# Performance work log

Hardware: AMD Instinct MI355X
Metric: run time of the kernel (lower is better)

## Reference

```python
import jax, jax.numpy as jnp
import numpy as np

B, S, H, NH = 2, 2048, 1024, 16
D = H // NH
EPS = 1.1920929e-07  # torch fp32 finfo eps used by F.rms_norm default
ROPE_BASE = 10000.0


def setup_inputs() -> dict:
    key = jax.random.key(0)
    k0, k1, k2, k3 = jax.random.split(key, 4)
    return {
        "x": jax.random.normal(k0, (B, S, H), jnp.float32),
        "ve": jax.random.normal(k1, (B, S, H), jnp.float32),
        "W_qkv": jax.random.normal(k2, (3 * H, H), jnp.float32) * 0.02,
        "W_o": jax.random.normal(k3, (H, H), jnp.float32) * 0.02,
        "lambdas": jnp.array([0.5, 0.5], jnp.float32),
    }


def _rms_norm(x):
    # F.rms_norm without learnable weight, over last dim
    return x * jax.lax.rsqrt(jnp.mean(x * x, axis=-1, keepdims=True) + EPS)


def _rope(x):
    # x: [b, s, h, d]; rotate-half style RoPE matching the Rotary module
    d = x.shape[-1]
    inv_freq = (1.0 / ROPE_BASE) ** (jnp.arange(0, d, 2, dtype=jnp.float32) / d)
    t = jnp.arange(x.shape[1], dtype=jnp.float32)
    freqs = t[:, None] * inv_freq[None, :]          # [s, d/2]
    cos = jnp.cos(freqs)[None, :, None, :]
    sin = jnp.sin(freqs)[None, :, None, :]
    x1, x2 = jnp.split(x, 2, axis=-1)
    return jnp.concatenate([x1 * cos + x2 * sin, -x1 * sin + x2 * cos], axis=-1)


def reference(x, ve, W_qkv, W_o, lambdas):
    qkv = x @ W_qkv.T                                # [b, s, 3H]
    q, k, v = jnp.split(qkv, 3, axis=-1)
    rs = lambda a: a.reshape(B, S, NH, D)            # b s (h d) -> b s h d
    q, k, v = rs(q), rs(k), rs(v)
    q = _rope(_rms_norm(q))
    k = _rope(_rms_norm(k))
    v = lambdas[0] * v + lambdas[1] * rs(ve)         # value-lambda mix
    scale = 1.0 / jnp.sqrt(jnp.asarray(D, jnp.float32))  # flex_attention default
    scores = jnp.einsum('bqhd,bkhd->bhqk', q, k) * scale
    causal = jnp.tril(jnp.ones((S, S), bool))
    scores = jnp.where(causal[None, None], scores, jnp.asarray(-jnp.inf, scores.dtype))
    p = jax.nn.softmax(scores, axis=-1)
    a = jnp.einsum('bhqk,bkhd->bqhd', p, v).reshape(B, S, H)
    return a @ W_o.T
```

## Files before the change

kernel.cpp:

```cpp
#include <hip/hip_runtime.h>
#include <math.h>

typedef __bf16 bf16;
typedef __attribute__((ext_vector_type(8))) __bf16 bf16x8;
typedef __attribute__((ext_vector_type(4))) __bf16 bf16x4;
typedef __attribute__((ext_vector_type(4))) float f32x4;

#define B_  2
#define S_  2048
#define H_  1024
#define NH_ 16
#define D_  64

__device__ __forceinline__ f32x4 mfma16(bf16x8 a, bf16x8 b, f32x4 c) {
    return __builtin_amdgcn_mfma_f32_16x16x32_bf16(a, b, c, 0, 0, 0);
}

__device__ __forceinline__ void async16(void* lds, const void* g) {
    __builtin_amdgcn_global_load_lds(
        (const __attribute__((address_space(1))) unsigned int*)g,
        (__attribute__((address_space(3))) unsigned int*)lds, 16, 0, 0);
}

__global__ __launch_bounds__(256) void cvt_main(
    const float* __restrict__ x, const float* __restrict__ wqkv,
    bf16* __restrict__ xb, bf16* __restrict__ wqb, float2* __restrict__ tab)
{
    const int bid = blockIdx.x, tid = threadIdx.x;
    if (bid < 4096) {
        int i = bid * 256 + tid;
        f32x4 v = *(const f32x4*)(x + (size_t)i * 4);
        bf16x4 o; o[0]=(bf16)v[0]; o[1]=(bf16)v[1]; o[2]=(bf16)v[2]; o[3]=(bf16)v[3];
        *(bf16x4*)(xb + (size_t)i * 4) = o;
    } else if (bid < 7168) {
        int i = (bid - 4096) * 256 + tid;
        f32x4 v = *(const f32x4*)(wqkv + (size_t)i * 4);
        bf16x4 o; o[0]=(bf16)v[0]; o[1]=(bf16)v[1]; o[2]=(bf16)v[2]; o[3]=(bf16)v[3];
        *(bf16x4*)(wqb + (size_t)i * 4) = o;
    } else {
        int idx = (bid - 7168) * 256 + tid;
        int s = idx >> 5, i = idx & 31;
        float f = exp2f((float)i * (-13.287712379549449f / 32.0f));
        float sn, cs;
        sincosf((float)s * f, &sn, &cs);
        tab[idx] = make_float2(cs, sn);
    }
}

__global__ __launch_bounds__(256) void cvt_bf16(const float* __restrict__ src,
                                                bf16* __restrict__ dst, int n4) {
    int i = blockIdx.x * 256 + threadIdx.x;
    if (i >= n4) return;
    f32x4 v = *(const f32x4*)(src + (size_t)i * 4);
    bf16x4 o; o[0]=(bf16)v[0]; o[1]=(bf16)v[1]; o[2]=(bf16)v[2]; o[3]=(bf16)v[3];
    *(bf16x4*)(dst + (size_t)i * 4) = o;
}

template <int EPI, int NT>
__global__ __launch_bounds__(256) void gemm_bt(
    const bf16* __restrict__ A, const bf16* __restrict__ W,
    int M, int N, int K,
    float* __restrict__ outF,
    bf16* __restrict__ qb, bf16* __restrict__ kb, bf16* __restrict__ vtb,
    const float* __restrict__ ve, const float* __restrict__ lambdas,
    const float2* __restrict__ tab)
{
    constexpr int JN = NT / 32;
    __shared__ bf16 Al[128][64];
    __shared__ bf16 Bl[NT][64];
    const int m0   = blockIdx.y * 128;
    const int n0   = blockIdx.x * NT;
    const int tid  = threadIdx.x;
    const int lane = tid & 63;
    const int w    = tid >> 6;
    const int quad = lane >> 4;
    const int l16  = lane & 15;
    const int wm   = (w >> 1) * 64;
    const int wn   = (w & 1) * (NT / 2);
    const int r8   = lane >> 3;
    const int cs   = ((lane & 7) ^ r8) * 8;

    const f32x4 Z4 = {0.f, 0.f, 0.f, 0.f};
    f32x4 acc[4][JN];
#pragma unroll
    for (int i = 0; i < 4; ++i)
#pragma unroll
        for (int j = 0; j < JN; ++j) acc[i][j] = Z4;

    for (int k0 = 0; k0 < K; k0 += 64) {
        {
            const bf16* gA = A + (size_t)(m0 + w * 32 + r8) * K + k0 + cs;
            async16(&Al[w * 32][0],      gA);
            async16(&Al[w * 32 + 8][0],  gA + (size_t)8  * K);
            async16(&Al[w * 32 + 16][0], gA + (size_t)16 * K);
            async16(&Al[w * 32 + 24][0], gA + (size_t)24 * K);
        }
        if constexpr (NT == 128) {
            const bf16* gB = W + (size_t)(n0 + w * 32 + r8) * K + k0 + cs;
            async16(&Bl[w * 32][0],      gB);
            async16(&Bl[w * 32 + 8][0],  gB + (size_t)8  * K);
            async16(&Bl[w * 32 + 16][0], gB + (size_t)16 * K);
            async16(&Bl[w * 32 + 24][0], gB + (size_t)24 * K);
        } else {
            const bf16* gB = W + (size_t)(n0 + w * 16 + r8) * K + k0 + cs;
            async16(&Bl[w * 16][0],     gB);
            async16(&Bl[w * 16 + 8][0], gB + (size_t)8 * K);
        }
        __syncthreads();
#pragma unroll
        for (int ks = 0; ks < 2; ++ks) {
            bf16x8 af[4], bfg[JN];
#pragma unroll
            for (int i = 0; i < 4; ++i)
                af[i] = *(const bf16x8*)
                    &Al[wm + i * 16 + l16][(((ks << 2) + quad) ^ (l16 & 7)) * 8];
#pragma unroll
            for (int j = 0; j < JN; ++j)
                bfg[j] = *(const bf16x8*)
                    &Bl[wn + j * 16 + l16][(((ks << 2) + quad) ^ (l16 & 7)) * 8];
#pragma unroll
            for (int i = 0; i < 4; ++i)
#pragma unroll
                for (int j = 0; j < JN; ++j)
                    acc[i][j] = mfma16(af[i], bfg[j], acc[i][j]);
        }
        __syncthreads();
    }

    if constexpr (EPI == 1) {
#pragma unroll
        for (int i = 0; i < 4; ++i)
#pragma unroll
            for (int j = 0; j < JN; ++j)
#pragma unroll
                for (int r = 0; r < 4; ++r) {
                    int m = m0 + wm + i * 16 + quad * 4 + r;
                    int n = n0 + wn + j * 16 + l16;
                    outF[(size_t)m * N + n] = acc[i][j][r];
                }
    } else {
        const int nbase = n0 + wn;
        const int which = nbase >> 10;
        const int h     = (nbase & (H_ - 1)) >> 6;
        if (which < 2) {
            bf16* dst = which ? kb : qb;
#pragma unroll
            for (int i = 0; i < 4; ++i) {
                float ss[4];
#pragma unroll
                for (int r = 0; r < 4; ++r)
                    ss[r] = acc[i][0][r] * acc[i][0][r] + acc[i][1][r] * acc[i][1][r]
                          + acc[i][2][r] * acc[i][2][r] + acc[i][3][r] * acc[i][3][r];
#pragma unroll
                for (int r = 0; r < 4; ++r) {
                    ss[r] += __shfl_xor(ss[r], 1);
                    ss[r] += __shfl_xor(ss[r], 2);
                    ss[r] += __shfl_xor(ss[r], 4);
                    ss[r] += __shfl_xor(ss[r], 8);
                }
#pragma unroll
                for (int r = 0; r < 4; ++r) {
                    int    m   = m0 + wm + i * 16 + quad * 4 + r;
                    int    bb  = m >> 11, s = m & (S_ - 1);
                    float  rms = rsqrtf(ss[r] * (1.0f / 64.0f) + 1.1920929e-07f);
                    float  x0 = acc[i][0][r] * rms, x1 = acc[i][1][r] * rms;
                    float  x2 = acc[i][2][r] * rms, x3 = acc[i][3][r] * rms;
                    float2 t0 = tab[(size_t)s * 32 + l16];
                    float2 t1 = tab[(size_t)s * 32 + 16 + l16];
                    bf16*  bp = dst + ((size_t)(bb * NH_ + h) * S_ + s) * D_;
                    bp[l16]      = (bf16)(x0 * t0.x + x2 * t0.y);
                    bp[16 + l16] = (bf16)(x1 * t1.x + x3 * t1.y);
                    bp[32 + l16] = (bf16)(x2 * t0.x - x0 * t0.y);
                    bp[48 + l16] = (bf16)(x3 * t1.x - x1 * t1.y);
                }
            }
        } else {
            const float l0 = lambdas[0], l1 = lambdas[1];
#pragma unroll
            for (int i = 0; i < 4; ++i) {
                const int m00 = m0 + wm + i * 16 + quad * 4;
                const int bb  = m00 >> 11, s = m00 & (S_ - 1);
#pragma unroll
                for (int j = 0; j < 4; ++j) {
                    const int d = j * 16 + l16;
                    bf16x4 pk;
#pragma unroll
                    for (int r = 0; r < 4; ++r) {
                        float vm = l0 * acc[i][j][r]
                                 + l1 * ve[(size_t)(m00 + r) * H_ + h * 64 + d];
                        pk[r] = (bf16)vm;
                    }
                    *(bf16x4*)&vtb[((size_t)(bb * NH_ + h) * D_ + d) * S_ + s] = pk;
                }
            }
        }
    }
}

__global__ __launch_bounds__(256) void attn(
    const bf16* __restrict__ Q, const bf16* __restrict__ Kg,
    const bf16* __restrict__ Vt, bf16* __restrict__ Og)
{
    __shared__ bf16 Kl[2][64][64];
    __shared__ bf16 Vl[2][64][64];
    __shared__ bf16 Pl[4][16][64];

    const int bh   = blockIdx.y;
    const int b    = bh >> 4;
    const int h    = bh & 15;
    const int tid  = threadIdx.x;
    const int lane = tid & 63;
    const int w    = tid >> 6;
    const int quad = lane >> 4;
    const int l16  = lane & 15;
    const int l7   = l16 & 7;

    const bf16* Qp = Q  + (size_t)bh * S_ * D_;
    const bf16* Kp = Kg + (size_t)bh * S_ * D_;
    const bf16* Vp = Vt + (size_t)bh * D_ * S_;

    const int srow = lane >> 3;
    const int schk = (lane & 7) ^ (lane >> 3);
    const f32x4 Z4 = {0.f, 0.f, 0.f, 0.f};
    const float C1 = 0.18033688011112042f;
    const float C2 = -11.541560327111707f;

    auto stage = [&](int p, int kb0) {
        const bf16* gK = Kp + (size_t)(kb0 + w * 16 + srow) * D_ + schk * 8;
        async16(&Kl[p][w * 16][0], gK);
        async16(&Kl[p][w * 16 + 8][0], gK + (size_t)8 * D_);
        const bf16* gV = Vp + (size_t)(w * 16 + srow) * S_ + kb0 + schk * 8;
        async16(&Vl[p][w * 16][0], gV);
        async16(&Vl[p][w * 16 + 8][0], gV + (size_t)8 * S_);
    };

    for (int half = 0; half < 2; ++half) {
        const int qt    = half ? (31 - blockIdx.x) : blockIdx.x;
        const int qbase = qt * 64 + w * 16;
        const int qi    = qbase + l16;

        bf16x8 qf0 = *(const bf16x8*)(Qp + (size_t)(qbase + l16) * D_ + quad * 8);
        bf16x8 qf1 = *(const bf16x8*)(Qp + (size_t)(qbase + l16) * D_ + 32 + quad * 8);

        f32x4 of[4];
#pragma unroll
        for (int dt = 0; dt < 4; ++dt) of[dt] = Z4;
        float lsum = 0.f;

        const int nch = qt + 1;
        __syncthreads();
        stage(0, 0);
        for (int c = 0; c < nch; ++c) {
            const int p   = c & 1;
            const int kb0 = c * 64;
            __syncthreads();
            if (c + 1 < nch) stage(p ^ 1, kb0 + 64);

            float ps = 0.f;
            if (c < qt) {
#pragma unroll
                for (int nt = 0; nt < 4; ++nt) {
                    bf16x8 kf0 = *(const bf16x8*)&Kl[p][nt * 16 + l16][(quad ^ l7) * 8];
                    bf16x8 kf1 = *(const bf16x8*)&Kl[p][nt * 16 + l16][((quad + 4) ^ l7) * 8];
                    f32x4 sacc = Z4;
                    sacc = mfma16(kf0, qf0, sacc);
                    sacc = mfma16(kf1, qf1, sacc);
                    bf16x4 pk;
#pragma unroll
                    for (int r = 0; r < 4; ++r) {
                        float pv = exp2f(fmaf(sacc[r], C1, C2));
                        ps += pv;
                        pk[r] = (bf16)pv;
                    }
                    *(bf16x4*)&Pl[w][l16][((nt * 2 + (quad >> 1)) ^ l7) * 8 + (quad & 1) * 4] = pk;
                }
            } else {
#pragma unroll
                for (int nt = 0; nt < 4; ++nt) {
                    bf16x8 kf0 = *(const bf16x8*)&Kl[p][nt * 16 + l16][(quad ^ l7) * 8];
                    bf16x8 kf1 = *(const bf16x8*)&Kl[p][nt * 16 + l16][((quad + 4) ^ l7) * 8];
                    f32x4 sacc = Z4;
                    sacc = mfma16(kf0, qf0, sacc);
                    sacc = mfma16(kf1, qf1, sacc);
                    bf16x4 pk;
#pragma unroll
                    for (int r = 0; r < 4; ++r) {
                        int   key = kb0 + nt * 16 + quad * 4 + r;
                        float pv  = (key <= qi) ? exp2f(fmaf(sacc[r], C1, C2)) : 0.f;
                        ps += pv;
                        pk[r] = (bf16)pv;
                    }
                    *(bf16x4*)&Pl[w][l16][((nt * 2 + (quad >> 1)) ^ l7) * 8 + (quad & 1) * 4] = pk;
                }
            }
            ps += __shfl_xor(ps, 16);
            ps += __shfl_xor(ps, 32);
            lsum += ps;

            bf16x8 pf0 = *(const bf16x8*)&Pl[w][l16][(quad ^ l7) * 8];
            bf16x8 pf1 = *(const bf16x8*)&Pl[w][l16][((quad + 4) ^ l7) * 8];
#pragma unroll
            for (int dt = 0; dt < 4; ++dt) {
                bf16x8 vf0 = *(const bf16x8*)&Vl[p][dt * 16 + l16][(quad ^ l7) * 8];
                bf16x8 vf1 = *(const bf16x8*)&Vl[p][dt * 16 + l16][((quad + 4) ^ l7) * 8];
                of[dt] = mfma16(pf0, vf0, of[dt]);
                of[dt] = mfma16(pf1, vf1, of[dt]);
            }
        }

#pragma unroll
        for (int r = 0; r < 4; ++r) {
            float ld = __shfl(lsum, quad * 4 + r);
            float rl = 1.0f / ld;
            int   qq = qbase + quad * 4 + r;
#pragma unroll
            for (int dt = 0; dt < 4; ++dt)
                Og[((size_t)(b * S_ + qq)) * H_ + h * D_ + dt * 16 + l16] =
                    (bf16)(of[dt][r] * rl);
        }
    }
}

extern "C" void kernel_launch(void* const* d_in, const int* in_sizes, int n_in,
                              void* d_out, int out_size, void* d_ws, size_t ws_size,
                              hipStream_t stream)
{
    const float* x       = (const float*)d_in[0];
    const float* ve      = (const float*)d_in[1];
    const float* Wqkv    = (const float*)d_in[2];
    const float* Wo      = (const float*)d_in[3];
    const float* lambdas = (const float*)d_in[4];
    float* out = (float*)d_out;

    char* od = (char*)d_out;
    char* ws = (char*)d_ws;
    const size_t MB = 1024 * 1024;
    bf16*   xb  = (bf16*)(od);
    bf16*   wqb = (bf16*)(od + 8 * MB);
    float2* tab = (float2*)(od + 14 * MB);
    bf16*   qb  = (bf16*)(ws);
    bf16*   kb  = (bf16*)(ws + 8 * MB);
    bf16*   vtb = (bf16*)(ws + 16 * MB);
    bf16*   ao  = (bf16*)(ws + 24 * MB);
    bf16*   wob = (bf16*)(ws);

    cvt_main<<<7424, 256, 0, stream>>>(x, Wqkv, xb, wqb, tab);
    gemm_bt<0, 128><<<dim3(24, 32), 256, 0, stream>>>(
        xb, wqb, B_ * S_, 3 * H_, H_, nullptr, qb, kb, vtb, ve, lambdas, (const float2*)tab);
    attn<<<dim3(16, B_ * NH_), 256, 0, stream>>>(qb, kb, vtb, ao);
    cvt_bf16<<<1024, 256, 0, stream>>>(Wo, wob, (H_ * H_) / 4);
    gemm_bt<1, 64><<<dim3(16, 32), 256, 0, stream>>>(
        ao, wob, B_ * S_, H_, H_, out, nullptr, nullptr, nullptr, nullptr, nullptr, nullptr);
}
```

Before: 208.1 us.

## Double-buffer GEMM K loop and fuse W_o fp32-to-bf16 conversion into output GEMM

Restructures the GEMM main loop to use two 32-wide K stages in LDS, prefetching the next tile while MFMAs run on the current one, with one barrier per iteration instead of two. The output projection GEMM now reads W_o in fp32 directly, converts it to bf16 in registers and stores it to LDS, which removes the separate conversion kernel launch. This trades a smaller K-step per iteration and redundant per-block W_o conversion for fewer barriers, load/compute overlap and one fewer launch.

```diff
diff --git a/kernel.cpp b/kernel.cpp
--- a/kernel.cpp
+++ b/kernel.cpp
@@ -47,18 +47,10 @@
     }
 }
 
-__global__ __launch_bounds__(256) void cvt_bf16(const float* __restrict__ src,
-                                                bf16* __restrict__ dst, int n4) {
-    int i = blockIdx.x * 256 + threadIdx.x;
-    if (i >= n4) return;
-    f32x4 v = *(const f32x4*)(src + (size_t)i * 4);
-    bf16x4 o; o[0]=(bf16)v[0]; o[1]=(bf16)v[1]; o[2]=(bf16)v[2]; o[3]=(bf16)v[3];
-    *(bf16x4*)(dst + (size_t)i * 4) = o;
-}
-
 template <int EPI, int NT>
 __global__ __launch_bounds__(256) void gemm_bt(
     const bf16* __restrict__ A, const bf16* __restrict__ W,
+    const float* __restrict__ Wf,
     int M, int N, int K,
     float* __restrict__ outF,
     bf16* __restrict__ qb, bf16* __restrict__ kb, bf16* __restrict__ vtb,
@@ -66,8 +58,8 @@
     const float2* __restrict__ tab)
 {
     constexpr int JN = NT / 32;
-    __shared__ bf16 Al[128][64];
-    __shared__ bf16 Bl[NT][64];
+    __shared__ bf16 Al[2][128][32];
+    __shared__ bf16 Bl[2][NT][32];
     const int m0   = blockIdx.y * 128;
     const int n0   = blockIdx.x * NT;
     const int tid  = threadIdx.x;
@@ -77,8 +69,10 @@
     const int l16  = lane & 15;
     const int wm   = (w >> 1) * 64;
     const int wn   = (w & 1) * (NT / 2);
-    const int r8   = lane >> 3;
-    const int cs   = ((lane & 7) ^ r8) * 8;
+    const int g    = lane >> 2;
+    const int achk = (lane & 3) ^ (g & 3) ^ (g >> 2);
+    const int br   = tid >> 2;
+    const int bphy = (tid & 3) ^ (br & 3) ^ ((br >> 2) & 3);
 
     const f32x4 Z4 = {0.f, 0.f, 0.f, 0.f};
     f32x4 acc[4][JN];
@@ -87,44 +81,65 @@
 #pragma unroll
         for (int j = 0; j < JN; ++j) acc[i][j] = Z4;
 
-    for (int k0 = 0; k0 < K; k0 += 64) {
-        {
-            const bf16* gA = A + (size_t)(m0 + w * 32 + r8) * K + k0 + cs;
-            async16(&Al[w * 32][0],      gA);
-            async16(&Al[w * 32 + 8][0],  gA + (size_t)8  * K);
-            async16(&Al[w * 32 + 16][0], gA + (size_t)16 * K);
-            async16(&Al[w * 32 + 24][0], gA + (size_t)24 * K);
-        }
-        if constexpr (NT == 128) {
-            const bf16* gB = W + (size_t)(n0 + w * 32 + r8) * K + k0 + cs;
-            async16(&Bl[w * 32][0],      gB);
-            async16(&Bl[w * 32 + 8][0],  gB + (size_t)8  * K);
-            async16(&Bl[w * 32 + 16][0], gB + (size_t)16 * K);
-            async16(&Bl[w * 32 + 24][0], gB + (size_t)24 * K);
-        } else {
-            const bf16* gB = W + (size_t)(n0 + w * 16 + r8) * K + k0 + cs;
-            async16(&Bl[w * 16][0],     gB);
-            async16(&Bl[w * 16 + 8][0], gB + (size_t)8 * K);
-        }
+    auto stageA = [&](int p, int k0) {
+        const bf16* gA = A + (size_t)(m0 + w * 32 + g) * K + k0 + achk * 8;
+        async16(&Al[p][w * 32][0],      gA);
+        async16(&Al[p][w * 32 + 16][0], gA + (size_t)16 * K);
+    };
+    auto stageB = [&](int p, int k0) {
+        const bf16* gB = W + (size_t)(n0 + w * 32 + g) * K + k0 + achk * 8;
+        async16(&Bl[p][w * 32][0],      gB);
+        async16(&Bl[p][w * 32 + 16][0], gB + (size_t)16 * K);
+    };
+
+    const int niter = K >> 5;
+    stageA(0, 0);
+    if constexpr (EPI == 0) stageB(0, 0);
+    else {
+        const float* src = Wf + (size_t)(n0 + br) * K + (tid & 3) * 8;
+        f32x4 f0 = *(const f32x4*)(src);
+        f32x4 f1 = *(const f32x4*)(src + 4);
+        bf16x8 v;
+#pragma unroll
+        for (int q = 0; q < 4; ++q) { v[q] = (bf16)f0[q]; v[4 + q] = (bf16)f1[q]; }
+        *(bf16x8*)&Bl[0][br][bphy * 8] = v;
+    }
+
+    const int fsw = (l16 & 3) ^ (l16 >> 2);
+    for (int c = 0; c < niter; ++c) {
+        const int p = c & 1;
         __syncthreads();
-#pragma unroll
-        for (int ks = 0; ks < 2; ++ks) {
-            bf16x8 af[4], bfg[JN];
-#pragma unroll
-            for (int i = 0; i < 4; ++i)
-                af[i] = *(const bf16x8*)
-                    &Al[wm + i * 16 + l16][(((ks << 2) + quad) ^ (l16 & 7)) * 8];
+        const int k1 = (c + 1) << 5;
+        f32x4 f0, f1;
+        if (c + 1 < niter) {
+            stageA(p ^ 1, k1);
+            if constexpr (EPI == 0) stageB(p ^ 1, k1);
+            else {
+                const float* src = Wf + (size_t)(n0 + br) * K + k1 + (tid & 3) * 8;
+                f0 = *(const f32x4*)(src);
+                f1 = *(const f32x4*)(src + 4);
+            }
+        }
+        bf16x8 af[4], bfg[JN];
+#pragma unroll
+        for (int i = 0; i < 4; ++i)
+            af[i] = *(const bf16x8*)&Al[p][wm + i * 16 + l16][(quad ^ fsw) * 8];
+#pragma unroll
+        for (int j = 0; j < JN; ++j)
+            bfg[j] = *(const bf16x8*)&Bl[p][wn + j * 16 + l16][(quad ^ fsw) * 8];
+#pragma unroll
+        for (int i = 0; i < 4; ++i)
 #pragma unroll
             for (int j = 0; j < JN; ++j)
-                bfg[j] = *(const bf16x8*)
-                    &Bl[wn + j * 16 + l16][(((ks << 2) + quad) ^ (l16 & 7)) * 8];
-#pragma unroll
-            for (int i = 0; i < 4; ++i)
-#pragma unroll
-                for (int j = 0; j < JN; ++j)
-                    acc[i][j] = mfma16(af[i], bfg[j], acc[i][j]);
-        }
-        __syncthreads();
+                acc[i][j] = mfma16(af[i], bfg[j], acc[i][j]);
+        if constexpr (EPI == 1) {
+            if (c + 1 < niter) {
+                bf16x8 v;
+#pragma unroll
+                for (int q = 0; q < 4; ++q) { v[q] = (bf16)f0[q]; v[4 + q] = (bf16)f1[q]; }
+                *(bf16x8*)&Bl[p ^ 1][br][bphy * 8] = v;
+            }
+        }
     }
 
     if constexpr (EPI == 1) {
@@ -342,13 +357,13 @@
     bf16*   kb  = (bf16*)(ws + 8 * MB);
     bf16*   vtb = (bf16*)(ws + 16 * MB);
     bf16*   ao  = (bf16*)(ws + 24 * MB);
-    bf16*   wob = (bf16*)(ws);
 
     cvt_main<<<7424, 256, 0, stream>>>(x, Wqkv, xb, wqb, tab);
     gemm_bt<0, 128><<<dim3(24, 32), 256, 0, stream>>>(
-        xb, wqb, B_ * S_, 3 * H_, H_, nullptr, qb, kb, vtb, ve, lambdas, (const float2*)tab);
+        xb, wqb, nullptr, B_ * S_, 3 * H_, H_, nullptr, qb, kb, vtb, ve, lambdas,
+        (const float2*)tab);
     attn<<<dim3(16, B_ * NH_), 256, 0, stream>>>(qb, kb, vtb, ao);
-    cvt_bf16<<<1024, 256, 0, stream>>>(Wo, wob, (H_ * H_) / 4);
     gemm_bt<1, 64><<<dim3(16, 32), 256, 0, stream>>>(
-        ao, wob, B_ * S_, H_, H_, out, nullptr, nullptr, nullptr, nullptr, nullptr, nullptr);
-}
+        ao, nullptr, Wo, B_ * S_, H_, H_, out, nullptr, nullptr, nullptr,
+        nullptr, nullptr, nullptr);
+}
```

Result: slower. 222.1 us (+6.7%).

## Fuse W_o bf16 conversion into output GEMM and double query tile per attention block

Applied to the files above, without the earlier changes.

Removes the standalone W_o conversion kernel by loading fp32 W_o tiles into registers inside the output-projection GEMM, converting them to bf16 and storing them into swizzled LDS, with the next tile prefetched after the barrier. The attention kernel now processes 128 query rows per block as two 64-row sub-tiles sharing each staged K/V chunk, halving K/V LDS staging per query. This halves the attention grid, reducing parallelism to one block per CU, and adds per-element mask checks on all chunks.

```diff
diff --git a/kernel.cpp b/kernel.cpp
--- a/kernel.cpp
+++ b/kernel.cpp
@@ -47,18 +47,10 @@
     }
 }
 
-__global__ __launch_bounds__(256) void cvt_bf16(const float* __restrict__ src,
-                                                bf16* __restrict__ dst, int n4) {
-    int i = blockIdx.x * 256 + threadIdx.x;
-    if (i >= n4) return;
-    f32x4 v = *(const f32x4*)(src + (size_t)i * 4);
-    bf16x4 o; o[0]=(bf16)v[0]; o[1]=(bf16)v[1]; o[2]=(bf16)v[2]; o[3]=(bf16)v[3];
-    *(bf16x4*)(dst + (size_t)i * 4) = o;
-}
-
 template <int EPI, int NT>
 __global__ __launch_bounds__(256) void gemm_bt(
     const bf16* __restrict__ A, const bf16* __restrict__ W,
+    const float* __restrict__ Wf,
     int M, int N, int K,
     float* __restrict__ outF,
     bf16* __restrict__ qb, bf16* __restrict__ kb, bf16* __restrict__ vtb,
@@ -79,6 +71,8 @@
     const int wn   = (w & 1) * (NT / 2);
     const int r8   = lane >> 3;
     const int cs   = ((lane & 7) ^ r8) * 8;
+    const int tr   = tid >> 2;
+    const int c2   = (tid & 3) * 2;
 
     const f32x4 Z4 = {0.f, 0.f, 0.f, 0.f};
     f32x4 acc[4][JN];
@@ -87,7 +81,18 @@
 #pragma unroll
         for (int j = 0; j < JN; ++j) acc[i][j] = Z4;
 
-    for (int k0 = 0; k0 < K; k0 += 64) {
+    f32x4 wreg[4];
+    if constexpr (EPI == 1) {
+        const float* src = Wf + (size_t)(n0 + tr) * K + c2 * 8;
+        wreg[0] = *(const f32x4*)(src);
+        wreg[1] = *(const f32x4*)(src + 4);
+        wreg[2] = *(const f32x4*)(src + 8);
+        wreg[3] = *(const f32x4*)(src + 12);
+    }
+
+    const int niter = K >> 6;
+    for (int it = 0; it < niter; ++it) {
+        const int k0 = it << 6;
         {
             const bf16* gA = A + (size_t)(m0 + w * 32 + r8) * K + k0 + cs;
             async16(&Al[w * 32][0],      gA);
@@ -95,18 +100,32 @@
             async16(&Al[w * 32 + 16][0], gA + (size_t)16 * K);
             async16(&Al[w * 32 + 24][0], gA + (size_t)24 * K);
         }
-        if constexpr (NT == 128) {
+        if constexpr (EPI == 0) {
             const bf16* gB = W + (size_t)(n0 + w * 32 + r8) * K + k0 + cs;
             async16(&Bl[w * 32][0],      gB);
             async16(&Bl[w * 32 + 8][0],  gB + (size_t)8  * K);
             async16(&Bl[w * 32 + 16][0], gB + (size_t)16 * K);
             async16(&Bl[w * 32 + 24][0], gB + (size_t)24 * K);
         } else {
-            const bf16* gB = W + (size_t)(n0 + w * 16 + r8) * K + k0 + cs;
-            async16(&Bl[w * 16][0],     gB);
-            async16(&Bl[w * 16 + 8][0], gB + (size_t)8 * K);
+            bf16x8 v0, v1;
+#pragma unroll
+            for (int q = 0; q < 4; ++q) {
+                v0[q] = (bf16)wreg[0][q]; v0[4 + q] = (bf16)wreg[1][q];
+                v1[q] = (bf16)wreg[2][q]; v1[4 + q] = (bf16)wreg[3][q];
+            }
+            *(bf16x8*)&Bl[tr][(c2 ^ (tr & 7)) * 8]       = v0;
+            *(bf16x8*)&Bl[tr][((c2 + 1) ^ (tr & 7)) * 8] = v1;
         }
         __syncthreads();
+        if constexpr (EPI == 1) {
+            if (it + 1 < niter) {
+                const float* src = Wf + (size_t)(n0 + tr) * K + k0 + 64 + c2 * 8;
+                wreg[0] = *(const f32x4*)(src);
+                wreg[1] = *(const f32x4*)(src + 4);
+                wreg[2] = *(const f32x4*)(src + 8);
+                wreg[3] = *(const f32x4*)(src + 12);
+            }
+        }
 #pragma unroll
         for (int ks = 0; ks < 2; ++ks) {
             bf16x8 af[4], bfg[JN];
@@ -235,19 +254,27 @@
     };
 
     for (int half = 0; half < 2; ++half) {
-        const int qt    = half ? (31 - blockIdx.x) : blockIdx.x;
-        const int qbase = qt * 64 + w * 16;
-        const int qi    = qbase + l16;
-
-        bf16x8 qf0 = *(const bf16x8*)(Qp + (size_t)(qbase + l16) * D_ + quad * 8);
-        bf16x8 qf1 = *(const bf16x8*)(Qp + (size_t)(qbase + l16) * D_ + 32 + quad * 8);
-
-        f32x4 of[4];
-#pragma unroll
-        for (int dt = 0; dt < 4; ++dt) of[dt] = Z4;
-        float lsum = 0.f;
-
-        const int nch = qt + 1;
+        const int qt    = half ? (15 - blockIdx.x) : blockIdx.x;
+        const int qbase = qt * 128;
+
+        bf16x8 qf[2][2];
+        int    qi[2];
+#pragma unroll
+        for (int qs = 0; qs < 2; ++qs) {
+            int qr = qbase + qs * 64 + w * 16 + l16;
+            qi[qs] = qr;
+            qf[qs][0] = *(const bf16x8*)(Qp + (size_t)qr * D_ + quad * 8);
+            qf[qs][1] = *(const bf16x8*)(Qp + (size_t)qr * D_ + 32 + quad * 8);
+        }
+
+        f32x4 of[2][4];
+#pragma unroll
+        for (int qs = 0; qs < 2; ++qs)
+#pragma unroll
+            for (int dt = 0; dt < 4; ++dt) of[qs][dt] = Z4;
+        float lsum[2] = {0.f, 0.f};
+
+        const int nch = 2 * qt + 2;
         __syncthreads();
         stage(0, 0);
         for (int c = 0; c < nch; ++c) {
@@ -256,68 +283,56 @@
             __syncthreads();
             if (c + 1 < nch) stage(p ^ 1, kb0 + 64);
 
-            float ps = 0.f;
-            if (c < qt) {
+#pragma unroll
+            for (int qs = 0; qs < 2; ++qs) {
+                if (qs == 0 && c == 2 * qt + 1) continue;
+                const int klim = (c == 2 * qt + qs) ? qi[qs] : 0x7fffffff;
+                float ps = 0.f;
 #pragma unroll
                 for (int nt = 0; nt < 4; ++nt) {
                     bf16x8 kf0 = *(const bf16x8*)&Kl[p][nt * 16 + l16][(quad ^ l7) * 8];
                     bf16x8 kf1 = *(const bf16x8*)&Kl[p][nt * 16 + l16][((quad + 4) ^ l7) * 8];
                     f32x4 sacc = Z4;
-                    sacc = mfma16(kf0, qf0, sacc);
-                    sacc = mfma16(kf1, qf1, sacc);
+                    sacc = mfma16(kf0, qf[qs][0], sacc);
+                    sacc = mfma16(kf1, qf[qs][1], sacc);
                     bf16x4 pk;
 #pragma unroll
                     for (int r = 0; r < 4; ++r) {
-                        float pv = exp2f(fmaf(sacc[r], C1, C2));
+                        int   key = kb0 + nt * 16 + quad * 4 + r;
+                        float pv  = (key <= klim) ? exp2f(fmaf(sacc[r], C1, C2)) : 0.f;
                         ps += pv;
                         pk[r] = (bf16)pv;
                     }
                     *(bf16x4*)&Pl[w][l16][((nt * 2 + (quad >> 1)) ^ l7) * 8 + (quad & 1) * 4] = pk;
                 }
-            } else {
-#pragma unroll
-                for (int nt = 0; nt < 4; ++nt) {
-                    bf16x8 kf0 = *(const bf16x8*)&Kl[p][nt * 16 + l16][(quad ^ l7) * 8];
-                    bf16x8 kf1 = *(const bf16x8*)&Kl[p][nt * 16 + l16][((quad + 4) ^ l7) * 8];
-                    f32x4 sacc = Z4;
-                    sacc = mfma16(kf0, qf0, sacc);
-                    sacc = mfma16(kf1, qf1, sacc);
-                    bf16x4 pk;
-#pragma unroll
-                    for (int r = 0; r < 4; ++r) {
-                        int   key = kb0 + nt * 16 + quad * 4 + r;
-                        float pv  = (key <= qi) ? exp2f(fmaf(sacc[r], C1, C2)) : 0.f;
-                        ps += pv;
-                        pk[r] = (bf16)pv;
-                    }
-                    *(bf16x4*)&Pl[w][l16][((nt * 2 + (quad >> 1)) ^ l7) * 8 + (quad & 1) * 4] = pk;
-                }
-            }
-            ps += __shfl_xor(ps, 16);
-            ps += __shfl_xor(ps, 32);
-            lsum += ps;
-
-            bf16x8 pf0 = *(const bf16x8*)&Pl[w][l16][(quad ^ l7) * 8];
-            bf16x8 pf1 = *(const bf16x8*)&Pl[w][l16][((quad + 4) ^ l7) * 8];
-#pragma unroll
-            for (int dt = 0; dt < 4; ++dt) {
-                bf16x8 vf0 = *(const bf16x8*)&Vl[p][dt * 16 + l16][(quad ^ l7) * 8];
-                bf16x8 vf1 = *(const bf16x8*)&Vl[p][dt * 16 + l16][((quad + 4) ^ l7) * 8];
-                of[dt] = mfma16(pf0, vf0, of[dt]);
-                of[dt] = mfma16(pf1, vf1, of[dt]);
-            }
-        }
-
-#pragma unroll
-        for (int r = 0; r < 4; ++r) {
-            float ld = __shfl(lsum, quad * 4 + r);
-            float rl = 1.0f / ld;
-            int   qq = qbase + quad * 4 + r;
-#pragma unroll
-            for (int dt = 0; dt < 4; ++dt)
-                Og[((size_t)(b * S_ + qq)) * H_ + h * D_ + dt * 16 + l16] =
-                    (bf16)(of[dt][r] * rl);
-        }
+                ps += __shfl_xor(ps, 16);
+                ps += __shfl_xor(ps, 32);
+                lsum[qs] += ps;
+
+                bf16x8 pf0 = *(const bf16x8*)&Pl[w][l16][(quad ^ l7) * 8];
+                bf16x8 pf1 = *(const bf16x8*)&Pl[w][l16][((quad + 4) ^ l7) * 8];
+#pragma unroll
+                for (int dt = 0; dt < 4; ++dt) {
+                    bf16x8 vf0 = *(const bf16x8*)&Vl[p][dt * 16 + l16][(quad ^ l7) * 8];
+                    bf16x8 vf1 = *(const bf16x8*)&Vl[p][dt * 16 + l16][((quad + 4) ^ l7) * 8];
+                    of[qs][dt] = mfma16(pf0, vf0, of[qs][dt]);
+                    of[qs][dt] = mfma16(pf1, vf1, of[qs][dt]);
+                }
+            }
+        }
+
+#pragma unroll
+        for (int qs = 0; qs < 2; ++qs)
+#pragma unroll
+            for (int r = 0; r < 4; ++r) {
+                float ld = __shfl(lsum[qs], quad * 4 + r);
+                float rl = 1.0f / ld;
+                int   qq = qbase + qs * 64 + w * 16 + quad * 4 + r;
+#pragma unroll
+                for (int dt = 0; dt < 4; ++dt)
+                    Og[((size_t)(b * S_ + qq)) * H_ + h * D_ + dt * 16 + l16] =
+                        (bf16)(of[qs][dt][r] * rl);
+            }
     }
 }
 
@@ -342,13 +357,13 @@
     bf16*   kb  = (bf16*)(ws + 8 * MB);
     bf16*   vtb = (bf16*)(ws + 16 * MB);
     bf16*   ao  = (bf16*)(ws + 24 * MB);
-    bf16*   wob = (bf16*)(ws);
 
     cvt_main<<<7424, 256, 0, stream>>>(x, Wqkv, xb, wqb, tab);
     gemm_bt<0, 128><<<dim3(24, 32), 256, 0, stream>>>(
-        xb, wqb, B_ * S_, 3 * H_, H_, nullptr, qb, kb, vtb, ve, lambdas, (const float2*)tab);
-    attn<<<dim3(16, B_ * NH_), 256, 0, stream>>>(qb, kb, vtb, ao);
-    cvt_bf16<<<1024, 256, 0, stream>>>(Wo, wob, (H_ * H_) / 4);
+        xb, wqb, nullptr, B_ * S_, 3 * H_, H_, nullptr, qb, kb, vtb, ve, lambdas,
+        (const float2*)tab);
+    attn<<<dim3(8, B_ * NH_), 256, 0, stream>>>(qb, kb, vtb, ao);
     gemm_bt<1, 64><<<dim3(16, 32), 256, 0, stream>>>(
-        ao, wob, B_ * S_, H_, H_, out, nullptr, nullptr, nullptr, nullptr, nullptr, nullptr);
-}
+        ao, nullptr, Wo, B_ * S_, H_, H_, out, nullptr, nullptr, nullptr,
+        nullptr, nullptr, nullptr);
+}
```

Result: slower. 232.9 us (+11.9%).

## Split attention key range across two blocks and add a combine kernel

Applied to the files above, without the earlier changes.

Splits each query tile's causal key range into two halves handled by separate blocks (split-K attention). This doubles the attention grid from 512 to 1024 blocks to improve occupancy across the CUs. The unnormalized partial outputs and row sums are written to scratch buffers, then summed and normalized by a new combine kernel. Because the softmax uses a fixed offset rather than a running max, the partials add directly. The cost is an extra launch and extra global traffic for the partial outputs, and the partials are rounded to bf16 before being combined.

```diff
diff --git a/kernel.cpp b/kernel.cpp
--- a/kernel.cpp
+++ b/kernel.cpp
@@ -199,13 +199,15 @@
 
 __global__ __launch_bounds__(256) void attn(
     const bf16* __restrict__ Q, const bf16* __restrict__ Kg,
-    const bf16* __restrict__ Vt, bf16* __restrict__ Og)
+    const bf16* __restrict__ Vt, bf16* __restrict__ opart,
+    float* __restrict__ lsumg)
 {
     __shared__ bf16 Kl[2][64][64];
     __shared__ bf16 Vl[2][64][64];
     __shared__ bf16 Pl[4][16][64];
 
-    const int bh   = blockIdx.y;
+    const int sz   = blockIdx.y;
+    const int bh   = blockIdx.z;
     const int b    = bh >> 4;
     const int h    = bh & 15;
     const int tid  = threadIdx.x;
@@ -218,6 +220,8 @@
     const bf16* Qp = Q  + (size_t)bh * S_ * D_;
     const bf16* Kp = Kg + (size_t)bh * S_ * D_;
     const bf16* Vp = Vt + (size_t)bh * D_ * S_;
+    bf16*  op = opart + (size_t)sz * (B_ * S_ * H_);
+    float* lp = lsumg + sz * (B_ * NH_ * S_);
 
     const int srow = lane >> 3;
     const int schk = (lane & 7) ^ (lane >> 3);
@@ -238,6 +242,10 @@
         const int qt    = half ? (31 - blockIdx.x) : blockIdx.x;
         const int qbase = qt * 64 + w * 16;
         const int qi    = qbase + l16;
+        const int nt    = qt + 1;
+        const int h0    = (nt + 1) >> 1;
+        const int c0    = sz ? h0 : 0;
+        const int c1    = sz ? nt : h0;
 
         bf16x8 qf0 = *(const bf16x8*)(Qp + (size_t)(qbase + l16) * D_ + quad * 8);
         bf16x8 qf1 = *(const bf16x8*)(Qp + (size_t)(qbase + l16) * D_ + 32 + quad * 8);
@@ -247,78 +255,82 @@
         for (int dt = 0; dt < 4; ++dt) of[dt] = Z4;
         float lsum = 0.f;
 
-        const int nch = qt + 1;
-        __syncthreads();
-        stage(0, 0);
-        for (int c = 0; c < nch; ++c) {
-            const int p   = c & 1;
-            const int kb0 = c * 64;
+        if (c0 < c1) {
             __syncthreads();
-            if (c + 1 < nch) stage(p ^ 1, kb0 + 64);
-
-            float ps = 0.f;
-            if (c < qt) {
-#pragma unroll
-                for (int nt = 0; nt < 4; ++nt) {
-                    bf16x8 kf0 = *(const bf16x8*)&Kl[p][nt * 16 + l16][(quad ^ l7) * 8];
-                    bf16x8 kf1 = *(const bf16x8*)&Kl[p][nt * 16 + l16][((quad + 4) ^ l7) * 8];
+            stage(0, c0 * 64);
+            for (int c = c0; c < c1; ++c) {
+                const int p   = (c - c0) & 1;
+                const int kb0 = c * 64;
+                __syncthreads();
+                if (c + 1 < c1) stage(p ^ 1, kb0 + 64);
+
+                const int klim = (c == nt - 1) ? qi : 0x7fffffff;
+                float ps = 0.f;
+#pragma unroll
+                for (int ntl = 0; ntl < 4; ++ntl) {
+                    bf16x8 kf0 = *(const bf16x8*)&Kl[p][ntl * 16 + l16][(quad ^ l7) * 8];
+                    bf16x8 kf1 = *(const bf16x8*)&Kl[p][ntl * 16 + l16][((quad + 4) ^ l7) * 8];
                     f32x4 sacc = Z4;
                     sacc = mfma16(kf0, qf0, sacc);
                     sacc = mfma16(kf1, qf1, sacc);
                     bf16x4 pk;
 #pragma unroll
                     for (int r = 0; r < 4; ++r) {
-                        float pv = exp2f(fmaf(sacc[r], C1, C2));
+                        int   key = kb0 + ntl * 16 + quad * 4 + r;
+                        float pv  = (key <= klim) ? exp2f(fmaf(sacc[r], C1, C2)) : 0.f;
                         ps += pv;
                         pk[r] = (bf16)pv;
                     }
-                    *(bf16x4*)&Pl[w][l16][((nt * 2 + (quad >> 1)) ^ l7) * 8 + (quad & 1) * 4] = pk;
-                }
-            } else {
-#pragma unroll
-                for (int nt = 0; nt < 4; ++nt) {
-                    bf16x8 kf0 = *(const bf16x8*)&Kl[p][nt * 16 + l16][(quad ^ l7) * 8];
-                    bf16x8 kf1 = *(const bf16x8*)&Kl[p][nt * 16 + l16][((quad + 4) ^ l7) * 8];
-                    f32x4 sacc = Z4;
-                    sacc = mfma16(kf0, qf0, sacc);
-                    sacc = mfma16(kf1, qf1, sacc);
-                    bf16x4 pk;
-#pragma unroll
-                    for (int r = 0; r < 4; ++r) {
-                        int   key = kb0 + nt * 16 + quad * 4 + r;
-                        float pv  = (key <= qi) ? exp2f(fmaf(sacc[r], C1, C2)) : 0.f;
-                        ps += pv;
-                        pk[r] = (bf16)pv;
-                    }
-                    *(bf16x4*)&Pl[w][l16][((nt * 2 + (quad >> 1)) ^ l7) * 8 + (quad & 1) * 4] = pk;
+                    *(bf16x4*)&Pl[w][l16][((ntl * 2 + (quad >> 1)) ^ l7) * 8 + (quad & 1) * 4] = pk;
+                }
+                ps += __shfl_xor(ps, 16);
+                ps += __shfl_xor(ps, 32);
+                lsum += ps;
+
+                bf16x8 pf0 = *(const bf16x8*)&Pl[w][l16][(quad ^ l7) * 8];
+                bf16x8 pf1 = *(const bf16x8*)&Pl[w][l16][((quad + 4) ^ l7) * 8];
+#pragma unroll
+                for (int dt = 0; dt < 4; ++dt) {
+                    bf16x8 vf0 = *(const bf16x8*)&Vl[p][dt * 16 + l16][(quad ^ l7) * 8];
+                    bf16x8 vf1 = *(const bf16x8*)&Vl[p][dt * 16 + l16][((quad + 4) ^ l7) * 8];
+                    of[dt] = mfma16(pf0, vf0, of[dt]);
+                    of[dt] = mfma16(pf1, vf1, of[dt]);
                 }
             }
-            ps += __shfl_xor(ps, 16);
-            ps += __shfl_xor(ps, 32);
-            lsum += ps;
-
-            bf16x8 pf0 = *(const bf16x8*)&Pl[w][l16][(quad ^ l7) * 8];
-            bf16x8 pf1 = *(const bf16x8*)&Pl[w][l16][((quad + 4) ^ l7) * 8];
-#pragma unroll
-            for (int dt = 0; dt < 4; ++dt) {
-                bf16x8 vf0 = *(const bf16x8*)&Vl[p][dt * 16 + l16][(quad ^ l7) * 8];
-                bf16x8 vf1 = *(const bf16x8*)&Vl[p][dt * 16 + l16][((quad + 4) ^ l7) * 8];
-                of[dt] = mfma16(pf0, vf0, of[dt]);
-                of[dt] = mfma16(pf1, vf1, of[dt]);
-            }
         }
 
 #pragma unroll
         for (int r = 0; r < 4; ++r) {
-            float ld = __shfl(lsum, quad * 4 + r);
-            float rl = 1.0f / ld;
-            int   qq = qbase + quad * 4 + r;
+            int qq = qbase + quad * 4 + r;
 #pragma unroll
             for (int dt = 0; dt < 4; ++dt)
-                Og[((size_t)(b * S_ + qq)) * H_ + h * D_ + dt * 16 + l16] =
-                    (bf16)(of[dt][r] * rl);
-        }
+                op[((size_t)(b * S_ + qq)) * H_ + h * D_ + dt * 16 + l16] =
+                    (bf16)of[dt][r];
+        }
+        if (lane < 16)
+            lp[bh * S_ + qbase + lane] = lsum;
     }
+}
+
+__global__ __launch_bounds__(256) void combine(
+    const bf16* __restrict__ opart, const float* __restrict__ lsumg,
+    bf16* __restrict__ ao)
+{
+    const int i  = blockIdx.x * 256 + threadIdx.x;
+    const int e0 = i * 8;
+    const int bb = e0 >> 21;
+    const int s  = (e0 >> 10) & (S_ - 1);
+    const int h  = (e0 & (H_ - 1)) >> 6;
+    const int bh = bb * NH_ + h;
+    float l = lsumg[bh * S_ + s] + lsumg[B_ * NH_ * S_ + bh * S_ + s];
+    float rl = 1.0f / l;
+    bf16x8 a = *(const bf16x8*)(opart + e0);
+    bf16x8 c = *(const bf16x8*)(opart + (size_t)(B_ * S_ * H_) + e0);
+    bf16x8 o;
+#pragma unroll
+    for (int j = 0; j < 8; ++j)
+        o[j] = (bf16)(((float)a[j] + (float)c[j]) * rl);
+    *(bf16x8*)(ao + e0) = o;
 }
 
 extern "C" void kernel_launch(void* const* d_in, const int* in_sizes, int n_in,
@@ -335,20 +347,25 @@
     char* od = (char*)d_out;
     char* ws = (char*)d_ws;
     const size_t MB = 1024 * 1024;
-    bf16*   xb  = (bf16*)(od);
-    bf16*   wqb = (bf16*)(od + 8 * MB);
-    float2* tab = (float2*)(od + 14 * MB);
-    bf16*   qb  = (bf16*)(ws);
-    bf16*   kb  = (bf16*)(ws + 8 * MB);
-    bf16*   vtb = (bf16*)(ws + 16 * MB);
-    bf16*   ao  = (bf16*)(ws + 24 * MB);
-    bf16*   wob = (bf16*)(ws);
+    bf16*   xb    = (bf16*)(od);
+    bf16*   wqb   = (bf16*)(od + 8 * MB);
+    float2* tab   = (float2*)(od + 14 * MB);
+    bf16*   opart = (bf16*)(od);
+    bf16*   qb    = (bf16*)(ws);
+    bf16*   kb    = (bf16*)(ws + 8 * MB);
+    bf16*   vtb   = (bf16*)(ws + 16 * MB);
+    float*  lsum  = (float*)(ws + 24 * MB);
+    bf16*   wob   = (bf16*)(ws + 24 * MB + 512 * 1024);
+    bf16*   ao    = (bf16*)(ws);
 
     cvt_main<<<7424, 256, 0, stream>>>(x, Wqkv, xb, wqb, tab);
     gemm_bt<0, 128><<<dim3(24, 32), 256, 0, stream>>>(
-        xb, wqb, B_ * S_, 3 * H_, H_, nullptr, qb, kb, vtb, ve, lambdas, (const float2*)tab);
-    attn<<<dim3(16, B_ * NH_), 256, 0, stream>>>(qb, kb, vtb, ao);
+        xb, wqb, B_ * S_, 3 * H_, H_, nullptr, qb, kb, vtb, ve, lambdas,
+        (const float2*)tab);
+    attn<<<dim3(16, 2, B_ * NH_), 256, 0, stream>>>(qb, kb, vtb, opart, lsum);
+    combine<<<(B_ * S_ * H_) / (256 * 8), 256, 0, stream>>>(opart, lsum, ao);
     cvt_bf16<<<1024, 256, 0, stream>>>(Wo, wob, (H_ * H_) / 4);
     gemm_bt<1, 64><<<dim3(16, 32), 256, 0, stream>>>(
-        ao, wob, B_ * S_, H_, H_, out, nullptr, nullptr, nullptr, nullptr, nullptr, nullptr);
-}
+        ao, wob, B_ * S_, H_, H_, out, nullptr, nullptr, nullptr,
+        nullptr, nullptr, nullptr);
+}
```

New measurement: 217.2 us. 4.4% more time.
